# Performance work log

Measured on AMD Instinct MI355X. Metric: run time of the kernel, lower is better.

Reference implementation:

```python
import jax, jax.numpy as jnp
import numpy as np

N_SKILLS = 1000
N_PROBLEMS = 20000
EMB = 256
TIME_LOG = 5.0
B, S = 32, 2048


def setup_inputs() -> dict:
    key = jax.random.key(0)
    ks = jax.random.split(key, 10)
    skills = jax.random.randint(ks[0], (B, S), 0, N_SKILLS, dtype=jnp.int64) if jax.config.jax_enable_x64 else jax.random.randint(ks[0], (B, S), 0, N_SKILLS, dtype=jnp.int32)
    problems = jax.random.randint(ks[1], (B, S), 0, N_PROBLEMS, dtype=skills.dtype)
    times = jnp.sort(jax.random.randint(ks[2], (B, S), 0, 10_000_000, dtype=skills.dtype), axis=-1)
    labels = jax.random.randint(ks[3], (B, S), 0, 2, dtype=skills.dtype)
    std = 0.01
    alpha_inter_W = std * jax.random.normal(ks[4], (2 * N_SKILLS, EMB), dtype=jnp.float32)
    alpha_skill_W = std * jax.random.normal(ks[5], (N_SKILLS, EMB), dtype=jnp.float32)
    beta_inter_W = std * jax.random.normal(ks[6], (2 * N_SKILLS, EMB), dtype=jnp.float32)
    beta_skill_W = std * jax.random.normal(ks[7], (N_SKILLS, EMB), dtype=jnp.float32)
    problem_base_W = std * jax.random.normal(ks[8], (N_PROBLEMS, 1), dtype=jnp.float32)
    skill_base_W = std * jax.random.normal(ks[9], (N_SKILLS, 1), dtype=jnp.float32)
    return {
        "skills": skills, "problems": problems, "times": times, "labels": labels,
        "alpha_inter_W": alpha_inter_W, "alpha_skill_W": alpha_skill_W,
        "beta_inter_W": beta_inter_W, "beta_skill_W": beta_skill_W,
        "problem_base_W": problem_base_W, "skill_base_W": skill_base_W,
    }


def reference(skills, problems, times, labels,
              alpha_inter_W, alpha_skill_W, beta_inter_W, beta_skill_W,
              problem_base_W, skill_base_W):
    n_skills = alpha_skill_W.shape[0]
    inters = skills + labels * n_skills  # [B,S]

    alpha_src = alpha_inter_W[inters]      # [B,S,E]
    alpha_tgt = alpha_skill_W[skills]      # [B,S,E]
    alphas = jnp.einsum("bse,bte->bst", alpha_src, alpha_tgt)  # [B,S,S]

    beta_src = beta_inter_W[inters]
    beta_tgt = beta_skill_W[skills]
    betas = jnp.einsum("bse,bte->bst", beta_src, beta_tgt)
    betas = jnp.clip(betas + 1.0, 0.0, 10.0)

    t = times.astype(jnp.float32) / 1000.0
    delta_t = jnp.abs(t[:, :, None] - t[:, None, :])
    delta_t = jnp.log(delta_t + 1e-10) / jnp.log(jnp.float32(TIME_LOG))

    cross = alphas * jnp.exp(-betas * delta_t)  # [B,S,S]

    seq_len = skills.shape[1]
    # original keeps strict upper triangle (source i strictly before target j)
    keep = jnp.triu(jnp.ones((seq_len, seq_len), dtype=cross.dtype), k=1)
    sum_t = jnp.sum(cross * keep[None], axis=-2)  # sum over source dim -> [B,S]

    problem_bias = problem_base_W[problems][..., 0]  # [B,S]
    skill_bias = skill_base_W[skills][..., 0]        # [B,S]
    h = problem_bias + skill_bias + sum_t
    return jax.nn.sigmoid(h)
```

## Files before the change

### kernel.cpp

```cpp
#include <hip/hip_runtime.h>
#include <hip/hip_bf16.h>
#include <stdint.h>

#define NSK   1000
#define EMB   256
#define BB    32
#define SS    2048
#define TI    128
#define TJ    64
#define NUNITB 272
#define BK    64
#define NCHUNK (EMB / BK)
#define LDSB  24576
#define SCALE_INV (1.0f / 4096.0f)

typedef float f32x16 __attribute__((ext_vector_type(16)));
typedef float f32x4  __attribute__((ext_vector_type(4)));
typedef long  longx2 __attribute__((ext_vector_type(2)));

#define OFF_AI8 0
#define OFF_BI8 (2 * NSK * EMB)
#define OFF_AS8 (4 * NSK * EMB)
#define OFF_BS8 (5 * NSK * EMB)
#define TOT8    (6 * NSK * EMB)

__global__ void cvt_tables(const float* __restrict__ ai, const float* __restrict__ bi,
                           const float* __restrict__ as_, const float* __restrict__ bs,
                           int* __restrict__ ws8, float* __restrict__ acc) {
    int g = blockIdx.x * 256 + threadIdx.x;
    if (g < BB * SS) acc[g] = 0.0f;
    if (g * 4 >= TOT8) return;
    int e = g * 4;
    const float* src; int off;
    if (e < OFF_AS8) { if (e < OFF_BI8) { src = ai;  off = e; }
                       else             { src = bi;  off = e - OFF_BI8; } }
    else             { if (e < OFF_BS8) { src = as_; off = e - OFF_AS8; }
                       else             { src = bs;  off = e - OFF_BS8; } }
    const float4 v = *(const float4*)(src + off);
    int lo = __builtin_amdgcn_cvt_pk_fp8_f32(v.x * 64.0f, v.y * 64.0f, 0, false);
    int wd = __builtin_amdgcn_cvt_pk_fp8_f32(v.z * 64.0f, v.w * 64.0f, lo, true);
    ws8[g] = wd;
}

__device__ __attribute__((noinline)) float dot256(const float* __restrict__ a,
                                                  const float* __restrict__ b) {
    float s = 0.0f;
#pragma unroll 8
    for (int k = 0; k < EMB; ++k) s += a[k] * b[k];
    return s;
}

__global__ __launch_bounds__(256, 2) void hawkes_unit(
    const int* __restrict__ skills, const int* __restrict__ times,
    const int* __restrict__ labels, const unsigned char* __restrict__ tab,
    const float* __restrict__ aiW_f, const float* __restrict__ asW_f,
    const float* __restrict__ biW_f, const float* __restrict__ bsW_f,
    float* __restrict__ acc)
{
    __shared__ __align__(16) char  sbuf[2 * LDSB];
    __shared__ __align__(16) float t_i[TI];
    __shared__ __align__(16) float t_j[TJ];
    __shared__ int   idx_i[TI];
    __shared__ int   idx_j[TJ];
    __shared__ float colsum[TJ];

    const int u  = blockIdx.x;
    const int b  = u / NUNITB;
    const int p  = u - b * NUNITB;
    int m = (int)sqrtf((float)p);
    while ((m + 1) * (m + 2) <= p) ++m;
    while (m * (m + 1) > p) --m;
    int jt, it;
    if (p >= (m + 1) * (m + 1)) { jt = 2 * m + 1; it = p - (m + 1) * (m + 1); }
    else                        { jt = 2 * m;     it = p - m * (m + 1); }
    const int j0 = jt * TJ, i0 = it * TI;
    const bool partial = (i0 + TI - 1 >= j0);

    const int tid = threadIdx.x;
    const int l   = tid & 63;
    const int w   = tid >> 6;
    const int wi  = w >> 1, wj = w & 1;
    const int lane31 = l & 31;
    const int khalf  = l >> 5;

    if (tid < TJ) {
        int j = j0 + tid;
        idx_j[tid] = skills[b * SS + j];
        t_j[tid]   = (float)times[b * SS + j] / 1000.0f;
        colsum[tid] = 0.0f;
    } else if (tid < TJ + TI) {
        int q = tid - TJ;
        int ii = i0 + q;
        idx_i[q] = skills[b * SS + ii] + labels[b * SS + ii] * NSK;
        t_i[q]   = (float)times[b * SS + ii] / 1000.0f;
    }
    __syncthreads();

    const float tjv = t_j[wj * 32 + lane31];
    const int   jl  = wj * 32 + lane31;

    const unsigned char* rowptr[3];
    int wo[3];
#pragma unroll
    for (int s = 0; s < 3; ++s) {
        int mm = w * 3 + s;
        int tabbase, ldsbase, row;
        if (mm < 8) {
            int mb = mm & 3;
            tabbase = (mm < 4) ? OFF_AI8 : OFF_BI8;
            ldsbase = ((mm < 4) ? 0 : 8192) + mb * 2048;
            row = idx_i[mb * 32 + (l >> 1)];
        } else {
            int mb = mm & 1;
            tabbase = (mm < 10) ? OFF_AS8 : OFF_BS8;
            ldsbase = ((mm < 10) ? 16384 : 20480) + mb * 2048;
            row = idx_j[mb * 32 + (l >> 1)];
        }
        rowptr[s] = tab + tabbase + (size_t)row * EMB + (l & 1) * 32;
        wo[s] = ldsbase + (l & 1) * 1024 + (l >> 1) * 8;
    }

#define LOADC(dst, c)                                                  \
    do { _Pragma("unroll")                                             \
        for (int s = 0; s < 3; ++s) {                                  \
            dst[s][0] = *(const longx2*)(rowptr[s] + (c) * BK);        \
            dst[s][1] = *(const longx2*)(rowptr[s] + (c) * BK + 16);   \
        }                                                              \
    } while (0)
#define WRITEC(src, buf)                                               \
    do { char* db = sbuf + (buf) * LDSB;                               \
        _Pragma("unroll")                                              \
        for (int s = 0; s < 3; ++s) {                                  \
            *(long*)(db + wo[s])             = src[s][0].x;            \
            *(long*)(db + wo[s] + 256)       = src[s][0].y;            \
            *(long*)(db + wo[s] + 512)       = src[s][1].x;            \
            *(long*)(db + wo[s] + 512 + 256) = src[s][1].y;            \
        }                                                              \
    } while (0)

    f32x16 accA[2], accB[2];
#pragma unroll
    for (int mi = 0; mi < 2; ++mi) { accA[mi] = 0.0f; accB[mi] = 0.0f; }

    longx2 sreg[3][2];
    LOADC(sreg, 0);
    WRITEC(sreg, 0);

    for (int c = 0; c < NCHUNK; ++c) {
        if (c + 1 < NCHUNK) LOADC(sreg, c + 1);
        __syncthreads();

        const char* sb = sbuf + (c & 1) * LDSB;
#pragma unroll
        for (int ks = 0; ks < 4; ++ks) {
            long fa[2], fb[2], ga, gb;
#pragma unroll
            for (int mi = 0; mi < 2; ++mi) {
                int mb = (wi * 2 + mi) * 2048 + ks * 512 + l * 8;
                fa[mi] = *(const long*)(sb + 0    + mb);
                fb[mi] = *(const long*)(sb + 8192 + mb);
            }
            {
                int nb = wj * 2048 + ks * 512 + l * 8;
                ga = *(const long*)(sb + 16384 + nb);
                gb = *(const long*)(sb + 20480 + nb);
            }
#pragma unroll
            for (int mi = 0; mi < 2; ++mi) {
                accA[mi] = __builtin_amdgcn_mfma_f32_32x32x16_fp8_fp8(
                    fa[mi], ga, accA[mi], 0, 0, 0);
                accB[mi] = __builtin_amdgcn_mfma_f32_32x32x16_fp8_fp8(
                    fb[mi], gb, accB[mi], 0, 0, 0);
            }
        }

        if (c + 1 < NCHUNK) WRITEC(sreg, (c + 1) & 1);
    }

    float csum = 0.0f;
#pragma unroll
    for (int mi = 0; mi < 2; ++mi) {
        const int rbase = (wi * 2 + mi) * 32 + 4 * khalf;
        f32x4 tiv[4];
#pragma unroll
        for (int q = 0; q < 4; ++q) tiv[q] = *(const f32x4*)(t_i + rbase + 8 * q);
#pragma unroll
        for (int r = 0; r < 16; ++r) {
            const int q = r >> 2, e = r & 3;
            const int il = rbase + 8 * q + e;
            if (partial && i0 + il >= j0 + jl) continue;
            float d = fabsf(tiv[q][e] - tjv);
            float alpha, braw;
            if (d == 0.0f) {
                alpha = dot256(aiW_f + (size_t)idx_i[il] * EMB,
                               asW_f + (size_t)idx_j[jl] * EMB) * 4096.0f;
                braw  = dot256(biW_f + (size_t)idx_i[il] * EMB,
                               bsW_f + (size_t)idx_j[jl] * EMB) * 4096.0f;
            } else {
                alpha = accA[mi][r];
                braw  = accB[mi][r];
            }
            float dl   = __builtin_amdgcn_logf(d + 1e-10f) * 0.6213349345596119f;
            float beta = braw * SCALE_INV + 1.0f;
            csum += alpha * __builtin_amdgcn_exp2f(-beta * dl);
        }
    }
    csum *= SCALE_INV;

    __syncthreads();
    csum += __shfl_xor(csum, 32);
    if (l < 32)
        atomicAdd(&colsum[wj * 32 + lane31], csum);
    __syncthreads();
    if (tid < TJ)
        atomicAdd(&acc[b * SS + j0 + tid], colsum[tid]);
}

__global__ void hawkes_final(const int* __restrict__ skills, const int* __restrict__ problems,
                             const float* __restrict__ pbW, const float* __restrict__ sbW,
                             float* __restrict__ out) {
    int i = blockIdx.x * 256 + threadIdx.x;
    if (i >= BB * SS) return;
    float h = pbW[problems[i]] + sbW[skills[i]] + out[i];
    out[i] = 1.0f / (1.0f + __builtin_amdgcn_exp2f(-h * 1.4426950408889634f));
}

extern "C" void kernel_launch(void* const* d_in, const int* in_sizes, int n_in,
                              void* d_out, int out_size, void* d_ws, size_t ws_size,
                              hipStream_t stream) {
    const int*   skills   = (const int*)d_in[0];
    const int*   problems = (const int*)d_in[1];
    const int*   times    = (const int*)d_in[2];
    const int*   labels   = (const int*)d_in[3];
    const float* aiW      = (const float*)d_in[4];
    const float* asW      = (const float*)d_in[5];
    const float* biW      = (const float*)d_in[6];
    const float* bsW      = (const float*)d_in[7];
    const float* pbW      = (const float*)d_in[8];
    const float* sbW      = (const float*)d_in[9];
    float* out = (float*)d_out;
    unsigned char* tab = (unsigned char*)d_ws;

    cvt_tables<<<(TOT8 / 4 + 255) / 256, 256, 0, stream>>>(aiW, biW, asW, bsW,
                                                           (int*)tab, out);
    hawkes_unit<<<BB * NUNITB, 256, 0, stream>>>(skills, times, labels, tab,
                                                 aiW, asW, biW, bsW, out);
    hawkes_final<<<(BB * SS + 255) / 256, 256, 0, stream>>>(skills, problems, pbW, sbW, out);
}
```

Before: 178.4 us.

## Give each wave a private LDS region to drop block-wide barriers in GEMM loop

Each wave now owns 32 rows of i and all 64 j columns and stages its own private copy of the fp8 operand slices in a per-wave LDS region. That removes the __syncthreads per chunk and the double buffering. The cost is that every wave reloads the j-side (skill) rows redundantly, giving more global and LDS traffic, and the LDS write/read order within a wave now relies on wave-level ordering. The epilogue is restructured to produce two column partial sums per wave.

New measurement: 192.9 us. +8.1%, slower.

```diff
diff --git a/kernel.cpp b/kernel.cpp
--- a/kernel.cpp
+++ b/kernel.cpp
@@ -11,7 +11,7 @@
 #define NUNITB 272
 #define BK    64
 #define NCHUNK (EMB / BK)
-#define LDSB  24576
+#define WLDS  12288
 #define SCALE_INV (1.0f / 4096.0f)
 
 typedef float f32x16 __attribute__((ext_vector_type(16)));
@@ -57,7 +57,7 @@
     const float* __restrict__ biW_f, const float* __restrict__ bsW_f,
     float* __restrict__ acc)
 {
-    __shared__ __align__(16) char  sbuf[2 * LDSB];
+    __shared__ __align__(16) char  sbuf[4 * WLDS];
     __shared__ __align__(16) float t_i[TI];
     __shared__ __align__(16) float t_j[TJ];
     __shared__ int   idx_i[TI];
@@ -79,7 +79,6 @@
     const int tid = threadIdx.x;
     const int l   = tid & 63;
     const int w   = tid >> 6;
-    const int wi  = w >> 1, wj = w & 1;
     const int lane31 = l & 31;
     const int khalf  = l >> 5;
 
@@ -96,121 +95,112 @@
     }
     __syncthreads();
 
-    const float tjv = t_j[wj * 32 + lane31];
-    const int   jl  = wj * 32 + lane31;
-
-    const unsigned char* rowptr[3];
-    int wo[3];
-#pragma unroll
-    for (int s = 0; s < 3; ++s) {
-        int mm = w * 3 + s;
-        int tabbase, ldsbase, row;
-        if (mm < 8) {
-            int mb = mm & 3;
-            tabbase = (mm < 4) ? OFF_AI8 : OFF_BI8;
-            ldsbase = ((mm < 4) ? 0 : 8192) + mb * 2048;
-            row = idx_i[mb * 32 + (l >> 1)];
-        } else {
-            int mb = mm & 1;
-            tabbase = (mm < 10) ? OFF_AS8 : OFF_BS8;
-            ldsbase = ((mm < 10) ? 16384 : 20480) + mb * 2048;
-            row = idx_j[mb * 32 + (l >> 1)];
-        }
-        rowptr[s] = tab + tabbase + (size_t)row * EMB + (l & 1) * 32;
-        wo[s] = ldsbase + (l & 1) * 1024 + (l >> 1) * 8;
+    uint32_t roff[6];
+    int      wo[6];
+    {
+        const int rr = l >> 1;
+        const int pc = (l & 1) * 32;
+        const int ri  = idx_i[w * 32 + rr];
+        const int rj0 = idx_j[rr], rj1 = idx_j[32 + rr];
+        roff[0] = OFF_AI8 + (uint32_t)ri  * EMB + pc;
+        roff[1] = OFF_BI8 + (uint32_t)ri  * EMB + pc;
+        roff[2] = OFF_AS8 + (uint32_t)rj0 * EMB + pc;
+        roff[3] = OFF_AS8 + (uint32_t)rj1 * EMB + pc;
+        roff[4] = OFF_BS8 + (uint32_t)rj0 * EMB + pc;
+        roff[5] = OFF_BS8 + (uint32_t)rj1 * EMB + pc;
+        const int wbase = w * WLDS + (l & 1) * 1024 + rr * 8;
+#pragma unroll
+        for (int s = 0; s < 6; ++s) wo[s] = wbase + s * 2048;
     }
 
 #define LOADC(dst, c)                                                  \
     do { _Pragma("unroll")                                             \
-        for (int s = 0; s < 3; ++s) {                                  \
-            dst[s][0] = *(const longx2*)(rowptr[s] + (c) * BK);        \
-            dst[s][1] = *(const longx2*)(rowptr[s] + (c) * BK + 16);   \
+        for (int s = 0; s < 6; ++s) {                                  \
+            dst[s][0] = *(const longx2*)(tab + roff[s] + (c) * BK);    \
+            dst[s][1] = *(const longx2*)(tab + roff[s] + (c) * BK + 16); \
         }                                                              \
     } while (0)
-#define WRITEC(src, buf)                                               \
-    do { char* db = sbuf + (buf) * LDSB;                               \
-        _Pragma("unroll")                                              \
-        for (int s = 0; s < 3; ++s) {                                  \
-            *(long*)(db + wo[s])             = src[s][0].x;            \
-            *(long*)(db + wo[s] + 256)       = src[s][0].y;            \
-            *(long*)(db + wo[s] + 512)       = src[s][1].x;            \
-            *(long*)(db + wo[s] + 512 + 256) = src[s][1].y;            \
+#define WRITEC(src)                                                    \
+    do { _Pragma("unroll")                                             \
+        for (int s = 0; s < 6; ++s) {                                  \
+            *(long*)(sbuf + wo[s])             = src[s][0].x;          \
+            *(long*)(sbuf + wo[s] + 256)       = src[s][0].y;          \
+            *(long*)(sbuf + wo[s] + 512)       = src[s][1].x;          \
+            *(long*)(sbuf + wo[s] + 512 + 256) = src[s][1].y;          \
         }                                                              \
     } while (0)
 
     f32x16 accA[2], accB[2];
 #pragma unroll
-    for (int mi = 0; mi < 2; ++mi) { accA[mi] = 0.0f; accB[mi] = 0.0f; }
-
-    longx2 sreg[3][2];
+    for (int cb = 0; cb < 2; ++cb) { accA[cb] = 0.0f; accB[cb] = 0.0f; }
+
+    longx2 sreg[6][2];
     LOADC(sreg, 0);
-    WRITEC(sreg, 0);
-
+
+    const char* wb = sbuf + w * WLDS;
     for (int c = 0; c < NCHUNK; ++c) {
+        WRITEC(sreg);
         if (c + 1 < NCHUNK) LOADC(sreg, c + 1);
-        __syncthreads();
-
-        const char* sb = sbuf + (c & 1) * LDSB;
+
 #pragma unroll
         for (int ks = 0; ks < 4; ++ks) {
-            long fa[2], fb[2], ga, gb;
-#pragma unroll
-            for (int mi = 0; mi < 2; ++mi) {
-                int mb = (wi * 2 + mi) * 2048 + ks * 512 + l * 8;
-                fa[mi] = *(const long*)(sb + 0    + mb);
-                fb[mi] = *(const long*)(sb + 8192 + mb);
+            const int ko = ks * 512 + l * 8;
+            long fa  = *(const long*)(wb + 0     + ko);
+            long fb  = *(const long*)(wb + 2048  + ko);
+            long ga0 = *(const long*)(wb + 4096  + ko);
+            long ga1 = *(const long*)(wb + 6144  + ko);
+            long gb0 = *(const long*)(wb + 8192  + ko);
+            long gb1 = *(const long*)(wb + 10240 + ko);
+            accA[0] = __builtin_amdgcn_mfma_f32_32x32x16_fp8_fp8(fa, ga0, accA[0], 0, 0, 0);
+            accA[1] = __builtin_amdgcn_mfma_f32_32x32x16_fp8_fp8(fa, ga1, accA[1], 0, 0, 0);
+            accB[0] = __builtin_amdgcn_mfma_f32_32x32x16_fp8_fp8(fb, gb0, accB[0], 0, 0, 0);
+            accB[1] = __builtin_amdgcn_mfma_f32_32x32x16_fp8_fp8(fb, gb1, accB[1], 0, 0, 0);
+        }
+    }
+
+    float csum0 = 0.0f, csum1 = 0.0f;
+    {
+        const int rbase = w * 32 + 4 * khalf;
+        f32x4 tiv[4];
+#pragma unroll
+        for (int q = 0; q < 4; ++q) tiv[q] = *(const f32x4*)(t_i + rbase + 8 * q);
+#pragma unroll
+        for (int cb = 0; cb < 2; ++cb) {
+            const int   jl  = cb * 32 + lane31;
+            const float tjv = t_j[jl];
+            float s = 0.0f;
+#pragma unroll
+            for (int r = 0; r < 16; ++r) {
+                const int q = r >> 2, e = r & 3;
+                const int il = rbase + 8 * q + e;
+                if (partial && i0 + il >= j0 + jl) continue;
+                float d = fabsf(tiv[q][e] - tjv);
+                float alpha, braw;
+                if (d == 0.0f) {
+                    alpha = dot256(aiW_f + (size_t)idx_i[il] * EMB,
+                                   asW_f + (size_t)idx_j[jl] * EMB) * 4096.0f;
+                    braw  = dot256(biW_f + (size_t)idx_i[il] * EMB,
+                                   bsW_f + (size_t)idx_j[jl] * EMB) * 4096.0f;
+                } else {
+                    alpha = (cb == 0) ? accA[0][r] : accA[1][r];
+                    braw  = (cb == 0) ? accB[0][r] : accB[1][r];
+                }
+                float dl   = __builtin_amdgcn_logf(d + 1e-10f) * 0.6213349345596119f;
+                float beta = braw * SCALE_INV + 1.0f;
+                s += alpha * __builtin_amdgcn_exp2f(-beta * dl);
             }
-            {
-                int nb = wj * 2048 + ks * 512 + l * 8;
-                ga = *(const long*)(sb + 16384 + nb);
-                gb = *(const long*)(sb + 20480 + nb);
-            }
-#pragma unroll
-            for (int mi = 0; mi < 2; ++mi) {
-                accA[mi] = __builtin_amdgcn_mfma_f32_32x32x16_fp8_fp8(
-                    fa[mi], ga, accA[mi], 0, 0, 0);
-                accB[mi] = __builtin_amdgcn_mfma_f32_32x32x16_fp8_fp8(
-                    fb[mi], gb, accB[mi], 0, 0, 0);
-            }
+            if (cb == 0) csum0 += s; else csum1 += s;
         }
-
-        if (c + 1 < NCHUNK) WRITEC(sreg, (c + 1) & 1);
-    }
-
-    float csum = 0.0f;
-#pragma unroll
-    for (int mi = 0; mi < 2; ++mi) {
-        const int rbase = (wi * 2 + mi) * 32 + 4 * khalf;
-        f32x4 tiv[4];
-#pragma unroll
-        for (int q = 0; q < 4; ++q) tiv[q] = *(const f32x4*)(t_i + rbase + 8 * q);
-#pragma unroll
-        for (int r = 0; r < 16; ++r) {
-            const int q = r >> 2, e = r & 3;
-            const int il = rbase + 8 * q + e;
-            if (partial && i0 + il >= j0 + jl) continue;
-            float d = fabsf(tiv[q][e] - tjv);
-            float alpha, braw;
-            if (d == 0.0f) {
-                alpha = dot256(aiW_f + (size_t)idx_i[il] * EMB,
-                               asW_f + (size_t)idx_j[jl] * EMB) * 4096.0f;
-                braw  = dot256(biW_f + (size_t)idx_i[il] * EMB,
-                               bsW_f + (size_t)idx_j[jl] * EMB) * 4096.0f;
-            } else {
-                alpha = accA[mi][r];
-                braw  = accB[mi][r];
-            }
-            float dl   = __builtin_amdgcn_logf(d + 1e-10f) * 0.6213349345596119f;
-            float beta = braw * SCALE_INV + 1.0f;
-            csum += alpha * __builtin_amdgcn_exp2f(-beta * dl);
-        }
-    }
-    csum *= SCALE_INV;
-
-    __syncthreads();
-    csum += __shfl_xor(csum, 32);
-    if (l < 32)
-        atomicAdd(&colsum[wj * 32 + lane31], csum);
+    }
+    csum0 *= SCALE_INV;
+    csum1 *= SCALE_INV;
+
+    csum0 += __shfl_xor(csum0, 32);
+    csum1 += __shfl_xor(csum1, 32);
+    if (l < 32) {
+        atomicAdd(&colsum[lane31], csum0);
+        atomicAdd(&colsum[32 + lane31], csum1);
+    }
     __syncthreads();
     if (tid < TJ)
         atomicAdd(&acc[b * SS + j0 + tid], colsum[tid]);
```
